# Optimization experiments

Measured on AMD Instinct MI355X. Metric: run time of the kernel, lower is better.

## Reference

```python
import jax, jax.numpy as jnp
import numpy as np

NUM_HEADS = 16
D_ATT = 64


def setup_inputs() -> dict:
    key = jax.random.key(0)
    ks = jax.random.split(key, 7)
    b, n, hd = 4, 2048, NUM_HEADS * 64  # input last dim = num_heads * per-head embed_dim
    Q_vec = jax.random.normal(ks[0], (b, n, hd), dtype=jnp.float32)
    K_vec = jax.random.normal(ks[1], (b, n, hd), dtype=jnp.float32)
    V_vec = jax.random.normal(ks[2], (b, n, hd), dtype=jnp.float32)
    # torch Linear weights: [out_features, in_features] = [d_attention, per_head_dim]
    W_Q = jax.random.normal(ks[3], (D_ATT, 64), dtype=jnp.float32) * 0.02
    W_K = jax.random.normal(ks[4], (D_ATT, 64), dtype=jnp.float32) * 0.02
    W_V = jax.random.normal(ks[5], (D_ATT, 64), dtype=jnp.float32) * 0.02
    mask = jax.random.bernoulli(ks[6], p=0.9, shape=(b, n))  # bool [b, n]
    return {"Q_vec": Q_vec, "K_vec": K_vec, "V_vec": V_vec,
            "W_Q": W_Q, "W_K": W_K, "W_V": W_V, "mask": mask}


def reference(Q_vec, K_vec, V_vec, W_Q, W_K, W_V, mask):
    b, n, _ = Q_vec.shape
    h = NUM_HEADS
    scaling = 1.0 / np.sqrt(D_ATT).astype(np.float32)

    def split_heads(x):  # b n (h d) -> b h n d
        return x.reshape(b, n, h, -1).transpose(0, 2, 1, 3)

    # Linear applied per-head (weights are [out, in]; y = x @ W^T)
    q = split_heads(Q_vec) @ W_Q.T  # [b,h,n,D_ATT]
    k = split_heads(K_vec) @ W_K.T
    v = split_heads(V_vec) @ W_V.T

    dots = jnp.einsum('bhid,bhjd->bhij', q, k) * scaling  # [b,h,n,n]
    pair_mask = mask[:, None, :] & mask[:, :, None]       # [b,n,n]
    mask_value = -jnp.finfo(dots.dtype).max
    dots = jnp.where(pair_mask[:, None, :, :], dots, mask_value)
    attn = jax.nn.softmax(dots, axis=-1)
    out = jnp.einsum('bhij,bhjd->bhid', attn, v)          # [b,h,n,D_ATT]
    return out.transpose(0, 2, 1, 3).reshape(b, n, h * D_ATT)
```

## Files before the change

### kernel.cpp

```cpp
#include <hip/hip_runtime.h>

#define B_  4
#define N_  2048
#define H_  16
#define HD_ 1024

typedef short  bf16x8 __attribute__((ext_vector_type(8)));
typedef short  bf16x4 __attribute__((ext_vector_type(4)));
typedef float  f32x4  __attribute__((ext_vector_type(4)));

static __device__ __forceinline__ unsigned short f2bf(float f) {
    unsigned int u = __builtin_bit_cast(unsigned int, f);
    u += 0x7FFFu + ((u >> 16) & 1u);
    return (unsigned short)(u >> 16);
}

static __device__ __forceinline__ unsigned rne_hi(float f) {
    unsigned u = __builtin_bit_cast(unsigned, f);
    return u + 0x7FFFu + ((u >> 16) & 1u);
}
static __device__ __forceinline__ unsigned f2bf2pack(float lo, float hi) {
    return __builtin_amdgcn_perm(rne_hi(hi), rne_hi(lo), 0x07060302u);
}

__global__ __launch_bounds__(256) void proj_kernel(
    const float* __restrict__ Qv, const float* __restrict__ Kv,
    const float* __restrict__ Vv, const float* __restrict__ WQ,
    const float* __restrict__ WK, const float* __restrict__ WV,
    unsigned short* __restrict__ qs, unsigned short* __restrict__ ks,
    unsigned short* __restrict__ vt)
{
    __shared__ __align__(16) unsigned short xb[64][72];
    __shared__ __align__(16) unsigned short Wb[64][72];
    unsigned short (*sb)[72] = xb;

    const int tid  = threadIdx.x;
    const int wq   = tid >> 6;
    const int lane = tid & 63;
    const int l15  = lane & 15;
    const int quad = lane >> 4;

    const int i0 = blockIdx.x * 64;
    const int h  = blockIdx.y;
    const int bz = blockIdx.z;
    const int b  = bz / 3;
    const int p  = bz - b * 3;

    const size_t inbase = ((size_t)b * N_ + i0) * HD_ + h * 64;
    const size_t bh     = (size_t)b * H_ + h;

    const float* W   = (p == 0) ? WQ : (p == 1) ? WK : WV;
    const float* inp = ((p == 0) ? Qv : (p == 1) ? Kv : Vv) + inbase;

    for (int v = tid; v < 1024; v += 256) {
        int tok = v >> 4, c4 = (v & 15) * 4;
        float4 f = *reinterpret_cast<const float4*>(inp + (size_t)tok * HD_ + c4);
        uint2 u;
        u.x = f2bf2pack(f.x, f.y);
        u.y = f2bf2pack(f.z, f.w);
        *reinterpret_cast<uint2*>(&xb[tok][c4]) = u;
        float4 g = *reinterpret_cast<const float4*>(W + (size_t)v * 4);
        uint2 w2;
        w2.x = f2bf2pack(g.x, g.y);
        w2.y = f2bf2pack(g.z, g.w);
        *reinterpret_cast<uint2*>(&Wb[tok][c4]) = w2;
    }
    __syncthreads();

    bf16x8 ax[2];
    #pragma unroll
    for (int kh = 0; kh < 2; ++kh)
        ax[kh] = *reinterpret_cast<const bf16x8*>(&xb[wq * 16 + l15][kh * 32 + quad * 8]);

    f32x4 C[4];
    #pragma unroll
    for (int t = 0; t < 4; ++t) {
        C[t] = f32x4{0.f, 0.f, 0.f, 0.f};
        #pragma unroll
        for (int kh = 0; kh < 2; ++kh) {
            bf16x8 bw = *reinterpret_cast<const bf16x8*>(&Wb[t * 16 + l15][kh * 32 + quad * 8]);
            C[t] = __builtin_amdgcn_mfma_f32_16x16x32_bf16(ax[kh], bw, C[t], 0, 0, 0);
        }
    }

    __syncthreads();

    if (p < 2) {
        const float scl = (p == 0) ? 0.180336880f : 1.f;
        #pragma unroll
        for (int t = 0; t < 4; ++t)
            #pragma unroll
            for (int r = 0; r < 4; ++r)
                sb[wq * 16 + quad * 4 + r][t * 16 + l15] = f2bf(C[t][r] * scl);
        __syncthreads();
        unsigned short* dst = ((p == 0) ? qs : ks) + ((size_t)bh * N_ + i0) * 64;
        for (int v = tid; v < 512; v += 256) {
            int row = v >> 3, c0 = (v & 7) * 8;
            *reinterpret_cast<uint4*>(dst + (size_t)row * 64 + c0) =
                *reinterpret_cast<const uint4*>(&sb[row][c0]);
        }
    } else {
        #pragma unroll
        for (int t = 0; t < 4; ++t) {
            uint2 u;
            u.x = f2bf2pack(C[t][0], C[t][1]);
            u.y = f2bf2pack(C[t][2], C[t][3]);
            *reinterpret_cast<uint2*>(&sb[t * 16 + l15][wq * 16 + quad * 4]) = u;
        }
        __syncthreads();
        unsigned short* vdst = vt + (size_t)bh * 64 * N_ + i0;
        for (int v = tid; v < 512; v += 256) {
            int d = v >> 3, c0 = (v & 7) * 8;
            *reinterpret_cast<uint4*>(vdst + (size_t)d * N_ + c0) =
                *reinterpret_cast<const uint4*>(&sb[d][c0]);
        }
    }
}

__global__ __launch_bounds__(256, 2) void attn_kernel(
    const unsigned short* __restrict__ qs, const unsigned short* __restrict__ ks,
    const unsigned short* __restrict__ vt, const int* __restrict__ maskp,
    float* __restrict__ out)
{
    __shared__ __align__(16) unsigned short Ks[64][72];
    __shared__ __align__(16) unsigned short Vt[64][68];
    __shared__ float kb[64];

    const int tid  = threadIdx.x;
    const int w    = tid >> 6;
    const int lane = tid & 63;
    const int l15  = lane & 15;
    const int quad = lane >> 4;

    const int i0 = blockIdx.x * 256;
    const int bh = blockIdx.y;
    const int b  = bh >> 4;
    const int h  = bh & 15;
    const int qrow0 = i0 + w * 64;

    bf16x8 aq[4][2];
    float  qm[4];
    #pragma unroll
    for (int rt = 0; rt < 4; ++rt) {
        const unsigned short* qrow = qs + ((size_t)bh * N_ + qrow0 + rt * 16 + l15) * 64;
        aq[rt][0] = *reinterpret_cast<const bf16x8*>(qrow + quad * 8);
        aq[rt][1] = *reinterpret_cast<const bf16x8*>(qrow + 32 + quad * 8);
        qm[rt] = maskp[b * N_ + qrow0 + rt * 16 + l15] ? 1.f : 0.f;
    }

    bf16x8 aones;
    #pragma unroll
    for (int j = 0; j < 8; ++j) aones[j] = (short)0x3F80;

    f32x4 O[4][4];
    f32x4 L[4];
    #pragma unroll
    for (int rt = 0; rt < 4; ++rt) {
        L[rt] = f32x4{0.f, 0.f, 0.f, 0.f};
        #pragma unroll
        for (int c = 0; c < 4; ++c) O[rt][c] = f32x4{0.f, 0.f, 0.f, 0.f};
    }

    const unsigned short* kbase = ks + (size_t)bh * N_ * 64;
    const unsigned short* vbase = vt + (size_t)bh * 64 * N_;

    for (int kv0 = 0; kv0 < N_; kv0 += 64) {
        __syncthreads();
        #pragma unroll
        for (int it = 0; it < 2; ++it) {
            int idx = tid + it * 256;
            int r = idx >> 3, g = idx & 7;
            *reinterpret_cast<uint4*>(&Ks[r][g * 8]) =
                *reinterpret_cast<const uint4*>(kbase + (size_t)(kv0 + r) * 64 + g * 8);
        }
        #pragma unroll
        for (int it = 0; it < 4; ++it) {
            int idx = tid + it * 256;
            int r = idx >> 4, g2 = idx & 15;
            *reinterpret_cast<uint2*>(&Vt[r][g2 * 4]) =
                *reinterpret_cast<const uint2*>(vbase + (size_t)r * N_ + kv0 + g2 * 4);
        }
        if (tid < 64) kb[tid] = maskp[b * N_ + kv0 + tid] ? 0.f : -1e30f;
        __syncthreads();

        bf16x8 ak[4][2];
        #pragma unroll
        for (int ct = 0; ct < 4; ++ct)
            #pragma unroll
            for (int kh = 0; kh < 2; ++kh)
                ak[ct][kh] = *reinterpret_cast<const bf16x8*>(&Ks[ct * 16 + l15][kh * 32 + quad * 8]);

        bf16x8 av[4][2];
        #pragma unroll
        for (int ct = 0; ct < 4; ++ct)
            #pragma unroll
            for (int kh = 0; kh < 2; ++kh) {
                bf16x4 lo = *reinterpret_cast<const bf16x4*>(&Vt[ct * 16 + l15][kh * 32 + quad * 4]);
                bf16x4 hi = *reinterpret_cast<const bf16x4*>(&Vt[ct * 16 + l15][kh * 32 + 16 + quad * 4]);
                av[ct][kh] = bf16x8{lo[0], lo[1], lo[2], lo[3], hi[0], hi[1], hi[2], hi[3]};
            }

        f32x4 kbv[4];
        #pragma unroll
        for (int ct = 0; ct < 4; ++ct)
            kbv[ct] = *reinterpret_cast<const f32x4*>(&kb[ct * 16 + quad * 4]);

        #pragma unroll
        for (int rt = 0; rt < 4; ++rt) {
            f32x4 S[4];
            #pragma unroll
            for (int ct = 0; ct < 4; ++ct) {
                S[ct] = kbv[ct];
                #pragma unroll
                for (int kh = 0; kh < 2; ++kh)
                    S[ct] = __builtin_amdgcn_mfma_f32_16x16x32_bf16(ak[ct][kh], aq[rt][kh], S[ct], 0, 0, 0);
            }
            unsigned pk[4][2];
            #pragma unroll
            for (int ct = 0; ct < 4; ++ct) {
                float e0 = __builtin_amdgcn_exp2f(S[ct][0] * qm[rt]);
                float e1 = __builtin_amdgcn_exp2f(S[ct][1] * qm[rt]);
                float e2 = __builtin_amdgcn_exp2f(S[ct][2] * qm[rt]);
                float e3 = __builtin_amdgcn_exp2f(S[ct][3] * qm[rt]);
                pk[ct][0] = f2bf2pack(e0, e1);
                pk[ct][1] = f2bf2pack(e2, e3);
            }
            bf16x8 ap[2];
            #pragma unroll
            for (int kh = 0; kh < 2; ++kh) {
                uint4 u = uint4{pk[2 * kh][0], pk[2 * kh][1], pk[2 * kh + 1][0], pk[2 * kh + 1][1]};
                ap[kh] = __builtin_bit_cast(bf16x8, u);
            }
            #pragma unroll
            for (int kh = 0; kh < 2; ++kh)
                L[rt] = __builtin_amdgcn_mfma_f32_16x16x32_bf16(aones, ap[kh], L[rt], 0, 0, 0);
            #pragma unroll
            for (int ct = 0; ct < 4; ++ct)
                #pragma unroll
                for (int kh = 0; kh < 2; ++kh)
                    O[rt][ct] = __builtin_amdgcn_mfma_f32_16x16x32_bf16(av[ct][kh], ap[kh], O[rt][ct], 0, 0, 0);
        }
    }

    #pragma unroll
    for (int rt = 0; rt < 4; ++rt) {
        float inv = 1.f / L[rt][0];
        float* orow = out + ((size_t)b * N_ + qrow0 + rt * 16 + l15) * HD_ + h * 64 + quad * 4;
        #pragma unroll
        for (int ct = 0; ct < 4; ++ct)
            #pragma unroll
            for (int r = 0; r < 4; ++r)
                orow[ct * 16 + r] = O[rt][ct][r] * inv;
    }
}

extern "C" void kernel_launch(void* const* d_in, const int* in_sizes, int n_in,
                              void* d_out, int out_size, void* d_ws, size_t ws_size,
                              hipStream_t stream)
{
    const float* Qv  = (const float*)d_in[0];
    const float* Kv  = (const float*)d_in[1];
    const float* Vv  = (const float*)d_in[2];
    const float* WQ  = (const float*)d_in[3];
    const float* WK  = (const float*)d_in[4];
    const float* WV  = (const float*)d_in[5];
    const int*   msk = (const int*)d_in[6];
    float* out = (float*)d_out;

    const size_t per = (size_t)B_ * H_ * N_ * 64;
    unsigned short* qsb = (unsigned short*)d_ws;
    unsigned short* ksb = qsb + per;
    unsigned short* vtb = ksb + per;

    proj_kernel<<<dim3(N_ / 64, H_, B_ * 3), 256, 0, stream>>>(Qv, Kv, Vv, WQ, WK, WV, qsb, ksb, vtb);
    attn_kernel<<<dim3(N_ / 256, B_ * H_), 256, 0, stream>>>(qsb, ksb, vtb, msk, out);
}
```

Baseline: 238.2 us.

## Prefetch projection tiles in registers, double attention block size, cheaper bf16 rounding

The projection kernel now handles 256 tokens per block. Its weights are held in registers, and input tiles are double-buffered straight from global memory into registers instead of being staged through shared memory. The attention kernel moves to 512 threads per block, with each wave covering 32 query rows instead of 64. This halves accumulator register pressure and lets more waves share each K/V tile load. The bf16 conversion drops round-to-nearest-even for a simpler round-half-up, which changes numerics slightly.

```diff
diff --git a/kernel.cpp b/kernel.cpp
--- a/kernel.cpp
+++ b/kernel.cpp
@@ -11,28 +11,22 @@
 
 static __device__ __forceinline__ unsigned short f2bf(float f) {
     unsigned int u = __builtin_bit_cast(unsigned int, f);
-    u += 0x7FFFu + ((u >> 16) & 1u);
-    return (unsigned short)(u >> 16);
-}
-
-static __device__ __forceinline__ unsigned rne_hi(float f) {
-    unsigned u = __builtin_bit_cast(unsigned, f);
-    return u + 0x7FFFu + ((u >> 16) & 1u);
+    return (unsigned short)((u + 0x8000u) >> 16);
 }
 static __device__ __forceinline__ unsigned f2bf2pack(float lo, float hi) {
-    return __builtin_amdgcn_perm(rne_hi(hi), rne_hi(lo), 0x07060302u);
-}
-
-__global__ __launch_bounds__(256) void proj_kernel(
+    unsigned a = __builtin_bit_cast(unsigned, lo) + 0x8000u;
+    unsigned b = __builtin_bit_cast(unsigned, hi) + 0x8000u;
+    return __builtin_amdgcn_perm(b, a, 0x07060302u);
+}
+
+__global__ __launch_bounds__(256, 4) void proj_kernel(
     const float* __restrict__ Qv, const float* __restrict__ Kv,
     const float* __restrict__ Vv, const float* __restrict__ WQ,
     const float* __restrict__ WK, const float* __restrict__ WV,
     unsigned short* __restrict__ qs, unsigned short* __restrict__ ks,
     unsigned short* __restrict__ vt)
 {
-    __shared__ __align__(16) unsigned short xb[64][72];
-    __shared__ __align__(16) unsigned short Wb[64][72];
-    unsigned short (*sb)[72] = xb;
+    __shared__ __align__(16) unsigned short sb[64][72];
 
     const int tid  = threadIdx.x;
     const int wq   = tid >> 6;
@@ -40,84 +34,105 @@
     const int l15  = lane & 15;
     const int quad = lane >> 4;
 
-    const int i0 = blockIdx.x * 64;
+    const int i0 = blockIdx.x * 256;
     const int h  = blockIdx.y;
     const int bz = blockIdx.z;
     const int b  = bz / 3;
     const int p  = bz - b * 3;
 
-    const size_t inbase = ((size_t)b * N_ + i0) * HD_ + h * 64;
-    const size_t bh     = (size_t)b * H_ + h;
-
+    const size_t bh = (size_t)b * H_ + h;
     const float* W   = (p == 0) ? WQ : (p == 1) ? WK : WV;
-    const float* inp = ((p == 0) ? Qv : (p == 1) ? Kv : Vv) + inbase;
-
-    for (int v = tid; v < 1024; v += 256) {
-        int tok = v >> 4, c4 = (v & 15) * 4;
-        float4 f = *reinterpret_cast<const float4*>(inp + (size_t)tok * HD_ + c4);
-        uint2 u;
-        u.x = f2bf2pack(f.x, f.y);
-        u.y = f2bf2pack(f.z, f.w);
-        *reinterpret_cast<uint2*>(&xb[tok][c4]) = u;
-        float4 g = *reinterpret_cast<const float4*>(W + (size_t)v * 4);
-        uint2 w2;
-        w2.x = f2bf2pack(g.x, g.y);
-        w2.y = f2bf2pack(g.z, g.w);
-        *reinterpret_cast<uint2*>(&Wb[tok][c4]) = w2;
-    }
-    __syncthreads();
-
-    bf16x8 ax[2];
-    #pragma unroll
-    for (int kh = 0; kh < 2; ++kh)
-        ax[kh] = *reinterpret_cast<const bf16x8*>(&xb[wq * 16 + l15][kh * 32 + quad * 8]);
-
-    f32x4 C[4];
-    #pragma unroll
-    for (int t = 0; t < 4; ++t) {
-        C[t] = f32x4{0.f, 0.f, 0.f, 0.f};
+    const float* inp = ((p == 0) ? Qv : (p == 1) ? Kv : Vv)
+                       + ((size_t)b * N_ + i0) * HD_ + h * 64;
+
+    bf16x8 bw[4][2];
+    #pragma unroll
+    for (int t = 0; t < 4; ++t)
         #pragma unroll
         for (int kh = 0; kh < 2; ++kh) {
-            bf16x8 bw = *reinterpret_cast<const bf16x8*>(&Wb[t * 16 + l15][kh * 32 + quad * 8]);
-            C[t] = __builtin_amdgcn_mfma_f32_16x16x32_bf16(ax[kh], bw, C[t], 0, 0, 0);
-        }
-    }
-
-    __syncthreads();
-
-    if (p < 2) {
-        const float scl = (p == 0) ? 0.180336880f : 1.f;
-        #pragma unroll
-        for (int t = 0; t < 4; ++t)
-            #pragma unroll
-            for (int r = 0; r < 4; ++r)
-                sb[wq * 16 + quad * 4 + r][t * 16 + l15] = f2bf(C[t][r] * scl);
-        __syncthreads();
-        unsigned short* dst = ((p == 0) ? qs : ks) + ((size_t)bh * N_ + i0) * 64;
-        for (int v = tid; v < 512; v += 256) {
-            int row = v >> 3, c0 = (v & 7) * 8;
-            *reinterpret_cast<uint4*>(dst + (size_t)row * 64 + c0) =
-                *reinterpret_cast<const uint4*>(&sb[row][c0]);
-        }
-    } else {
-        #pragma unroll
-        for (int t = 0; t < 4; ++t) {
-            uint2 u;
-            u.x = f2bf2pack(C[t][0], C[t][1]);
-            u.y = f2bf2pack(C[t][2], C[t][3]);
-            *reinterpret_cast<uint2*>(&sb[t * 16 + l15][wq * 16 + quad * 4]) = u;
-        }
-        __syncthreads();
-        unsigned short* vdst = vt + (size_t)bh * 64 * N_ + i0;
-        for (int v = tid; v < 512; v += 256) {
-            int d = v >> 3, c0 = (v & 7) * 8;
-            *reinterpret_cast<uint4*>(vdst + (size_t)d * N_ + c0) =
-                *reinterpret_cast<const uint4*>(&sb[d][c0]);
-        }
-    }
-}
-
-__global__ __launch_bounds__(256, 2) void attn_kernel(
+            const float* wp = W + (size_t)(t * 16 + l15) * 64 + kh * 32 + quad * 8;
+            float4 f0 = *reinterpret_cast<const float4*>(wp);
+            float4 f1 = *reinterpret_cast<const float4*>(wp + 4);
+            uint4 u = uint4{f2bf2pack(f0.x, f0.y), f2bf2pack(f0.z, f0.w),
+                            f2bf2pack(f1.x, f1.y), f2bf2pack(f1.z, f1.w)};
+            bw[t][kh] = __builtin_bit_cast(bf16x8, u);
+        }
+
+    const float scl = (p == 0) ? 0.180336880f : 1.f;
+    unsigned short* dst  = ((p == 0) ? qs : ks) + ((size_t)bh * N_ + i0) * 64;
+    unsigned short* vdst = vt + (size_t)bh * 64 * N_ + i0;
+
+#define LOAD_X(st, XR) {                                                          \
+        const float* xp = inp + (size_t)((st) * 64 + wq * 16 + l15) * HD_;        \
+        XR[0] = *reinterpret_cast<const float4*>(xp + quad * 8);                  \
+        XR[1] = *reinterpret_cast<const float4*>(xp + quad * 8 + 4);              \
+        XR[2] = *reinterpret_cast<const float4*>(xp + 32 + quad * 8);             \
+        XR[3] = *reinterpret_cast<const float4*>(xp + 32 + quad * 8 + 4);         \
+    }
+
+#define DO_TILE(st, XR, FIRST) {                                                  \
+        bf16x8 ax0, ax1;                                                          \
+        { uint4 u = uint4{f2bf2pack(XR[0].x, XR[0].y), f2bf2pack(XR[0].z, XR[0].w),\
+                          f2bf2pack(XR[1].x, XR[1].y), f2bf2pack(XR[1].z, XR[1].w)};\
+          ax0 = __builtin_bit_cast(bf16x8, u); }                                  \
+        { uint4 u = uint4{f2bf2pack(XR[2].x, XR[2].y), f2bf2pack(XR[2].z, XR[2].w),\
+                          f2bf2pack(XR[3].x, XR[3].y), f2bf2pack(XR[3].z, XR[3].w)};\
+          ax1 = __builtin_bit_cast(bf16x8, u); }                                  \
+        f32x4 C[4];                                                               \
+        _Pragma("unroll")                                                         \
+        for (int t = 0; t < 4; ++t) {                                             \
+            C[t] = f32x4{0.f, 0.f, 0.f, 0.f};                                     \
+            C[t] = __builtin_amdgcn_mfma_f32_16x16x32_bf16(ax0, bw[t][0], C[t], 0, 0, 0); \
+            C[t] = __builtin_amdgcn_mfma_f32_16x16x32_bf16(ax1, bw[t][1], C[t], 0, 0, 0); \
+        }                                                                         \
+        if (!(FIRST)) __syncthreads();   \
+        if (p < 2) {                                                              \
+            _Pragma("unroll")                                                     \
+            for (int t = 0; t < 4; ++t)                                           \
+                _Pragma("unroll")                                                 \
+                for (int r = 0; r < 4; ++r)                                       \
+                    sb[wq * 16 + quad * 4 + r][t * 16 + l15] = f2bf(C[t][r] * scl); \
+            __syncthreads();                                                      \
+            _Pragma("unroll")                                                     \
+            for (int v = 0; v < 2; ++v) {                                         \
+                int idx = tid + v * 256;                                          \
+                int row = idx >> 3, c0 = (idx & 7) * 8;                           \
+                *reinterpret_cast<uint4*>(dst + (size_t)((st) * 64 + row) * 64 + c0) = \
+                    *reinterpret_cast<const uint4*>(&sb[row][c0]);                \
+            }                                                                     \
+        } else {                                                                  \
+            _Pragma("unroll")                                                     \
+            for (int t = 0; t < 4; ++t) {                                         \
+                uint2 u;                                                          \
+                u.x = f2bf2pack(C[t][0], C[t][1]);                                \
+                u.y = f2bf2pack(C[t][2], C[t][3]);                                \
+                *reinterpret_cast<uint2*>(&sb[t * 16 + l15][wq * 16 + quad * 4]) = u; \
+            }                                                                     \
+            __syncthreads();                                                      \
+            _Pragma("unroll")                                                     \
+            for (int v = 0; v < 2; ++v) {                                         \
+                int idx = tid + v * 256;                                          \
+                int d = idx >> 3, c0 = (idx & 7) * 8;                             \
+                *reinterpret_cast<uint4*>(vdst + (size_t)d * N_ + (st) * 64 + c0) = \
+                    *reinterpret_cast<const uint4*>(&sb[d][c0]);                  \
+            }                                                                     \
+        }                                                                         \
+    }
+
+    float4 x0[4], x1[4];
+    LOAD_X(0, x0);
+    LOAD_X(1, x1);
+    DO_TILE(0, x0, true);
+    LOAD_X(2, x0);
+    DO_TILE(1, x1, false);
+    LOAD_X(3, x1);
+    DO_TILE(2, x0, false);
+    DO_TILE(3, x1, false);
+#undef LOAD_X
+#undef DO_TILE
+}
+
+__global__ __launch_bounds__(512, 4) void attn_kernel(
     const unsigned short* __restrict__ qs, const unsigned short* __restrict__ ks,
     const unsigned short* __restrict__ vt, const int* __restrict__ maskp,
     float* __restrict__ out)
@@ -136,12 +151,12 @@
     const int bh = blockIdx.y;
     const int b  = bh >> 4;
     const int h  = bh & 15;
-    const int qrow0 = i0 + w * 64;
-
-    bf16x8 aq[4][2];
-    float  qm[4];
-    #pragma unroll
-    for (int rt = 0; rt < 4; ++rt) {
+    const int qrow0 = i0 + w * 32;
+
+    bf16x8 aq[2][2];
+    float  qm[2];
+    #pragma unroll
+    for (int rt = 0; rt < 2; ++rt) {
         const unsigned short* qrow = qs + ((size_t)bh * N_ + qrow0 + rt * 16 + l15) * 64;
         aq[rt][0] = *reinterpret_cast<const bf16x8*>(qrow + quad * 8);
         aq[rt][1] = *reinterpret_cast<const bf16x8*>(qrow + 32 + quad * 8);
@@ -152,10 +167,10 @@
     #pragma unroll
     for (int j = 0; j < 8; ++j) aones[j] = (short)0x3F80;
 
-    f32x4 O[4][4];
-    f32x4 L[4];
-    #pragma unroll
-    for (int rt = 0; rt < 4; ++rt) {
+    f32x4 O[2][4];
+    f32x4 L[2];
+    #pragma unroll
+    for (int rt = 0; rt < 2; ++rt) {
         L[rt] = f32x4{0.f, 0.f, 0.f, 0.f};
         #pragma unroll
         for (int c = 0; c < 4; ++c) O[rt][c] = f32x4{0.f, 0.f, 0.f, 0.f};
@@ -166,16 +181,14 @@
 
     for (int kv0 = 0; kv0 < N_; kv0 += 64) {
         __syncthreads();
-        #pragma unroll
-        for (int it = 0; it < 2; ++it) {
-            int idx = tid + it * 256;
-            int r = idx >> 3, g = idx & 7;
+        {
+            int r = tid >> 3, g = tid & 7;
             *reinterpret_cast<uint4*>(&Ks[r][g * 8]) =
                 *reinterpret_cast<const uint4*>(kbase + (size_t)(kv0 + r) * 64 + g * 8);
         }
         #pragma unroll
-        for (int it = 0; it < 4; ++it) {
-            int idx = tid + it * 256;
+        for (int it = 0; it < 2; ++it) {
+            int idx = tid + it * 512;
             int r = idx >> 4, g2 = idx & 15;
             *reinterpret_cast<uint2*>(&Vt[r][g2 * 4]) =
                 *reinterpret_cast<const uint2*>(vbase + (size_t)r * N_ + kv0 + g2 * 4);
@@ -206,7 +219,7 @@
             kbv[ct] = *reinterpret_cast<const f32x4*>(&kb[ct * 16 + quad * 4]);
 
         #pragma unroll
-        for (int rt = 0; rt < 4; ++rt) {
+        for (int rt = 0; rt < 2; ++rt) {
             f32x4 S[4];
             #pragma unroll
             for (int ct = 0; ct < 4; ++ct) {
@@ -243,7 +256,7 @@
     }
 
     #pragma unroll
-    for (int rt = 0; rt < 4; ++rt) {
+    for (int rt = 0; rt < 2; ++rt) {
         float inv = 1.f / L[rt][0];
         float* orow = out + ((size_t)b * N_ + qrow0 + rt * 16 + l15) * HD_ + h * 64 + quad * 4;
         #pragma unroll
@@ -272,6 +285,6 @@
     unsigned short* ksb = qsb + per;
     unsigned short* vtb = ksb + per;
 
-    proj_kernel<<<dim3(N_ / 64, H_, B_ * 3), 256, 0, stream>>>(Qv, Kv, Vv, WQ, WK, WV, qsb, ksb, vtb);
-    attn_kernel<<<dim3(N_ / 256, B_ * H_), 256, 0, stream>>>(qsb, ksb, vtb, msk, out);
-}
+    proj_kernel<<<dim3(N_ / 256, H_, B_ * 3), 256, 0, stream>>>(Qv, Kv, Vv, WQ, WK, WV, qsb, ksb, vtb);
+    attn_kernel<<<dim3(N_ / 256, B_ * H_), 512, 0, stream>>>(qsb, ksb, vtb, msk, out);
+}
```

Result: slower. 419.6 us (+76.2%).
